# Kernel optimization log

Measured on AMD Instinct MI355X. Metric: run time of the kernel, lower is better.

The kernel has to match this reference:

```python
import jax, jax.numpy as jnp
import numpy as np

B, N_ATOM, N_TOK = 1, 1536, 384
C_ATOM, C_PAIR, C_TOK = 128, 16, 384
C_HID, H, L = 32, 4, 3
HID = 2 * C_ATOM  # n_transition = 2
N_QUERY, N_KEY, INF = 32, 128, 1e9


def _ln(x, gamma=None, beta=None, eps=1e-5):
    mu = jnp.mean(x, axis=-1, keepdims=True)
    var = jnp.mean(jnp.square(x - mu), axis=-1, keepdims=True)
    y = (x - mu) * jax.lax.rsqrt(var + eps)
    if gamma is not None:
        y = y * gamma
    if beta is not None:
        y = y + beta
    return y


def _adaln(a, s, gamma_s, Wg, bg, Ws):
    an = _ln(a)            # LN without affine
    sn = _ln(s, gamma_s)   # scale-only LN
    return jax.nn.sigmoid(sn @ Wg + bg) * an + sn @ Ws


def _block_mask():
    # AtomTransformer.forward: 32-query x 128-key block-local mask
    offset = N_QUERY // 2 - 0.5
    n_center = N_ATOM // N_QUERY + 1
    centers = offset + jnp.arange(n_center, dtype=jnp.float32) * N_QUERY
    idx = jnp.arange(N_ATOM, dtype=jnp.float32)[:, None]
    row = (jnp.abs(idx - centers[None, :]) < N_QUERY / 2).astype(jnp.float32)
    col = (jnp.abs(idx - centers[None, :]) < N_KEY / 2).astype(jnp.float32)
    return (row @ col.T - 1.0) * INF   # [N,N]: 0 in-window, -INF outside


def _forward(ref_pos, ref_mask, ref_element, ref_charge, ref_atom_name_chars,
             ref_space_uid, token_mask, atom_to_token_index,
             W_feats, W_ref_offset, W_inv_sq, W_valid, W_l, W_m,
             W_mlp1, W_mlp2, W_mlp3, W_out_tok,
             attn_ada_gamma_s, attn_ada_Wg, attn_ada_bg, attn_ada_Ws,
             Wq, bq, Wk, Wv, lnz_g, lnz_b, Wb, Wgate, Wo, Wsg, bsg,
             tr_ada_gamma_s, tr_ada_Wg, tr_ada_bg, tr_ada_Ws,
             tr_W1, tr_W2, tr_Wog, tr_bog, tr_Wout):
    # --- RefAtomFeatureEmbedder (AF3 Alg 5 lines 1-6) ---
    feats = jnp.concatenate([
        ref_pos, ref_mask[..., None], ref_element, ref_charge[..., None],
        ref_atom_name_chars.reshape(B, N_ATOM, -1), ref_space_uid[..., None]], axis=-1)
    cl = feats @ W_feats                                     # [B,N,C_ATOM]
    d = ref_pos[:, None, :, :] - ref_pos[:, :, None, :]      # d[l,m] = pos[m]-pos[l]
    v = (ref_space_uid[:, None, :] == ref_space_uid[:, :, None]).astype(jnp.float32)[..., None]
    plm = (d @ W_ref_offset) * v
    inv_sq = 1.0 / (1.0 + jnp.sum(d * d, axis=-1, keepdims=True))
    plm = plm + (inv_sq @ W_inv_sq) * v + (v @ W_valid) * v  # [B,N,N,C_PAIR]
    ql = cl
    # --- single -> pair conditioning + pair MLP ---
    crelu = jax.nn.relu(cl)
    plm = plm + (crelu @ W_l)[:, :, None, :] + (crelu @ W_m)[:, None, :, :]
    h = jax.nn.relu(plm) @ W_mlp1
    h = jax.nn.relu(h) @ W_mlp2
    h = jax.nn.relu(h) @ W_mlp3
    plm = plm + h
    # --- AtomTransformer (Alg 7) -> DiffusionTransformer (Alg 23) ---
    beta = _block_mask()                                     # [N,N]
    atom_mask = jnp.einsum('blt,bt->bl', atom_to_token_index, token_mask)
    mask_bias = (atom_mask - 1.0)[:, None, None, :] * INF    # [B,1,1,N]
    a, s = ql, cl
    inv_sqrt = 1.0 / np.sqrt(C_HID)
    for i in range(L):
        # AttentionPairBias (Alg 24)
        an = _adaln(a, s, attn_ada_gamma_s[i], attn_ada_Wg[i], attn_ada_bg[i], attn_ada_Ws[i])
        q = (an @ Wq[i] + bq[i]).reshape(B, N_ATOM, H, C_HID)
        k = (an @ Wk[i]).reshape(B, N_ATOM, H, C_HID)
        vv = (an @ Wv[i]).reshape(B, N_ATOM, H, C_HID)
        zb = _ln(plm, lnz_g[i], lnz_b[i]) @ Wb[i]            # [B,N,N,H]
        logits = (jnp.einsum('bqhc,bkhc->bhqk', q, k) * inv_sqrt
                  + jnp.moveaxis(zb, -1, 1) + beta[None, None] + mask_bias)
        A = jax.nn.softmax(logits, axis=-1)
        o = jnp.einsum('bhqk,bkhc->bqhc', A, vv)
        g = jax.nn.sigmoid(an @ Wgate[i]).reshape(B, N_ATOM, H, C_HID)
        o = (g * o).reshape(B, N_ATOM, H * C_HID) @ Wo[i]
        attn_out = jax.nn.sigmoid(s @ Wsg[i] + bsg[i]) * o
        # ConditionedTransitionBlock (Alg 25) on pre-attention a (Alg 23)
        tn = _adaln(a, s, tr_ada_gamma_s[i], tr_ada_Wg[i], tr_ada_bg[i], tr_ada_Ws[i])
        hh = jax.nn.silu(tn @ tr_W1[i]) * (tn @ tr_W2[i])
        tr_out = jax.nn.sigmoid(s @ tr_Wog[i] + tr_bog[i]) * (hh @ tr_Wout[i])
        a = attn_out + tr_out
    # --- mean-aggregate atoms -> tokens (Alg 5 line 15) ---
    al = jax.nn.relu(a @ W_out_tok)                          # [B,N,C_TOK]
    counts = jnp.maximum(jnp.sum(atom_to_token_index, axis=1), 1.0)
    a_tok = jnp.einsum('blt,blc->btc', atom_to_token_index, al) / counts[..., None]
    return a_tok


def setup_inputs() -> dict:
    key = jax.random.key(0)
    ks = iter(jax.random.split(key, 80))

    def nrm(shape, scale=0.02):
        return jax.random.normal(next(ks), shape, dtype=jnp.float32) * scale

    inp = {}
    inp['ref_pos'] = jax.random.normal(next(ks), (B, N_ATOM, 3), dtype=jnp.float32) * 3.0
    inp['ref_mask'] = jnp.ones((B, N_ATOM), jnp.float32)
    elem = jax.random.randint(next(ks), (B, N_ATOM), 0, 128)
    inp['ref_element'] = jax.nn.one_hot(elem, 128, dtype=jnp.float32)
    inp['ref_charge'] = jax.random.normal(next(ks), (B, N_ATOM), dtype=jnp.float32)
    chars = jax.random.randint(next(ks), (B, N_ATOM, 4), 0, 64)
    inp['ref_atom_name_chars'] = jax.nn.one_hot(chars, 64, dtype=jnp.float32)
    inp['ref_space_uid'] = jnp.broadcast_to(
        (jnp.arange(N_ATOM) // 8).astype(jnp.float32), (B, N_ATOM))
    inp['token_mask'] = jnp.ones((B, N_TOK), jnp.float32)
    tok = (jnp.arange(N_ATOM) * N_TOK) // N_ATOM  # ~4 atoms per token
    inp['atom_to_token_index'] = jnp.broadcast_to(
        jax.nn.one_hot(tok, N_TOK, dtype=jnp.float32), (B, N_ATOM, N_TOK))
    # embedder params
    inp['W_feats'] = nrm((390, C_ATOM))
    inp['W_ref_offset'] = nrm((3, C_PAIR))
    inp['W_inv_sq'] = nrm((1, C_PAIR))
    inp['W_valid'] = nrm((1, C_PAIR))
    inp['W_l'] = nrm((C_ATOM, C_PAIR))
    inp['W_m'] = nrm((C_ATOM, C_PAIR))
    inp['W_mlp1'] = nrm((C_PAIR, C_PAIR))
    inp['W_mlp2'] = nrm((C_PAIR, C_PAIR))
    inp['W_mlp3'] = nrm((C_PAIR, C_PAIR))
    inp['W_out_tok'] = nrm((C_ATOM, C_TOK))
    # DiffusionTransformer params, stacked over L blocks
    inp['attn_ada_gamma_s'] = jnp.ones((L, C_ATOM), jnp.float32)
    inp['attn_ada_Wg'] = nrm((L, C_ATOM, C_ATOM))
    inp['attn_ada_bg'] = jnp.zeros((L, C_ATOM), jnp.float32)
    inp['attn_ada_Ws'] = nrm((L, C_ATOM, C_ATOM))
    inp['Wq'] = nrm((L, C_ATOM, H * C_HID))
    inp['bq'] = jnp.zeros((L, H * C_HID), jnp.float32)
    inp['Wk'] = nrm((L, C_ATOM, H * C_HID))
    inp['Wv'] = nrm((L, C_ATOM, H * C_HID))
    inp['lnz_g'] = jnp.ones((L, C_PAIR), jnp.float32)
    inp['lnz_b'] = jnp.zeros((L, C_PAIR), jnp.float32)
    inp['Wb'] = nrm((L, C_PAIR, H))
    inp['Wgate'] = nrm((L, C_ATOM, H * C_HID))
    inp['Wo'] = nrm((L, H * C_HID, C_ATOM))
    inp['Wsg'] = nrm((L, C_ATOM, C_ATOM))
    inp['bsg'] = jnp.full((L, C_ATOM), -2.0, jnp.float32)
    inp['tr_ada_gamma_s'] = jnp.ones((L, C_ATOM), jnp.float32)
    inp['tr_ada_Wg'] = nrm((L, C_ATOM, C_ATOM))
    inp['tr_ada_bg'] = jnp.zeros((L, C_ATOM), jnp.float32)
    inp['tr_ada_Ws'] = nrm((L, C_ATOM, C_ATOM))
    inp['tr_W1'] = nrm((L, C_ATOM, HID))
    inp['tr_W2'] = nrm((L, C_ATOM, HID))
    inp['tr_Wog'] = nrm((L, C_ATOM, C_ATOM))
    inp['tr_bog'] = jnp.full((L, C_ATOM), -2.0, jnp.float32)
    inp['tr_Wout'] = nrm((L, HID, C_ATOM))
    return inp


def reference(ref_pos, ref_mask, ref_element, ref_charge, ref_atom_name_chars,
              ref_space_uid, token_mask, atom_to_token_index,
              W_feats, W_ref_offset, W_inv_sq, W_valid, W_l, W_m,
              W_mlp1, W_mlp2, W_mlp3, W_out_tok,
              attn_ada_gamma_s, attn_ada_Wg, attn_ada_bg, attn_ada_Ws,
              Wq, bq, Wk, Wv, lnz_g, lnz_b, Wb, Wgate, Wo, Wsg, bsg,
              tr_ada_gamma_s, tr_ada_Wg, tr_ada_bg, tr_ada_Ws,
              tr_W1, tr_W2, tr_Wog, tr_bog, tr_Wout):
    return _forward(ref_pos, ref_mask, ref_element, ref_charge, ref_atom_name_chars,
                    ref_space_uid, token_mask, atom_to_token_index,
                    W_feats, W_ref_offset, W_inv_sq, W_valid, W_l, W_m,
                    W_mlp1, W_mlp2, W_mlp3, W_out_tok,
                    attn_ada_gamma_s, attn_ada_Wg, attn_ada_bg, attn_ada_Ws,
                    Wq, bq, Wk, Wv, lnz_g, lnz_b, Wb, Wgate, Wo, Wsg, bsg,
                    tr_ada_gamma_s, tr_ada_Wg, tr_ada_bg, tr_ada_Ws,
                    tr_W1, tr_W2, tr_Wog, tr_bog, tr_Wout)
```

## Files before the change

kernel.cpp:

```cpp
#include <hip/hip_runtime.h>
#include <math.h>

#define N_ATOM 1536
#define NLAYER 3
#define NC     196608L
#define ZSTRIDE 786432L

struct GD { const float* A; const float* B; float* C; const float* ks; const float* bias;
            const float* sg; const float* ad; int act; int ldb; int ldc; int mode; };
struct GB { GD g[18]; };

__global__ __launch_bounds__(128) void embed_tok_kernel(
    const float* __restrict__ pos, const float* __restrict__ rmask,
    const float* __restrict__ elem, const float* __restrict__ charge,
    const float* __restrict__ chars, const float* __restrict__ uid,
    const float* __restrict__ Wf, const float* __restrict__ W_l, const float* __restrict__ W_m,
    const float* __restrict__ a2t, const float* __restrict__ tmask,
    float* __restrict__ cl, float* __restrict__ aa,
    float* __restrict__ pl, float* __restrict__ pm,
    int* __restrict__ tok, float* __restrict__ amask)
{
  int l = blockIdx.x, c = threadIdx.x;
  __shared__ int sidx[6];
  __shared__ float crow[128];
  if (elem[(long)l * 128 + c] > 0.5f) sidx[0] = c;
  float v0 = chars[(long)l * 256 + c];
  if (v0 > 0.5f) sidx[1 + (c >> 6)] = c & 63;
  float v1 = chars[(long)l * 256 + 128 + c];
  if (v1 > 0.5f) sidx[3 + (c >> 6)] = c & 63;
  for (int j = c; j < 384; j += 128)
    if (a2t[(long)l * 384 + j] > 0.5f) sidx[5] = j;
  __syncthreads();
  float acc = pos[l * 3 + 0] * Wf[c]
            + pos[l * 3 + 1] * Wf[128 + c]
            + pos[l * 3 + 2] * Wf[256 + c]
            + rmask[l] * Wf[384 + c]
            + Wf[(4 + sidx[0]) * 128 + c]
            + charge[l] * Wf[132 * 128 + c]
            + Wf[(133 + sidx[1]) * 128 + c]
            + Wf[(197 + sidx[2]) * 128 + c]
            + Wf[(261 + sidx[3]) * 128 + c]
            + Wf[(325 + sidx[4]) * 128 + c]
            + uid[l] * Wf[389 * 128 + c];
  long gi = (long)l * 128 + c;
  cl[gi] = acc; aa[gi] = acc; crow[c] = fmaxf(acc, 0.f);
  __syncthreads();
  if (c < 32) {
    const float* W = (c < 16) ? W_l : W_m;
    int o = c & 15;
    float s = 0.f;
    for (int cc = 0; cc < 128; cc++) s = fmaf(crow[cc], W[cc * 16 + o], s);
    if (c < 16) pl[l * 16 + o] = s; else pm[l * 16 + o] = s;
  }
  if (c == 127) {
    int j = sidx[5];
    tok[l] = j; amask[l] = tmask[j];
  }
}

__device__ __forceinline__ void gemm64_body(float* sm, const GD d, int row0, int col0) {
  float* As = sm; float* Bs = sm + 2176;
  float* rmu = sm + 4352;
  float* rsd = sm + 4416;
  int tid = threadIdx.x;
  if (d.mode >= 1) {
    int r = tid >> 2, sgi = tid & 3;
    const float* Ar = d.A + (long)(row0 + r) * 128 + sgi * 32;
    float4 vv[8];
    float s1 = 0.f;
#pragma unroll
    for (int c4 = 0; c4 < 8; c4++) {
      vv[c4] = *(const float4*)(Ar + c4 * 4);
      s1 += vv[c4].x + vv[c4].y + vv[c4].z + vv[c4].w;
    }
    s1 += __shfl_xor(s1, 1); s1 += __shfl_xor(s1, 2);
    float mu = s1 * (1.f / 128.f);
    float s2 = 0.f;
#pragma unroll
    for (int c4 = 0; c4 < 8; c4++) {
      float dx = vv[c4].x - mu, dy = vv[c4].y - mu, dz = vv[c4].z - mu, dw = vv[c4].w - mu;
      s2 += dx * dx + dy * dy + dz * dz + dw * dw;
    }
    s2 += __shfl_xor(s2, 1); s2 += __shfl_xor(s2, 2);
    if (sgi == 0) {
      rmu[r] = mu;
      rsd[r] = rsqrtf(s2 * (1.f / 128.f) + 1e-5f);
    }
  }
  int tx = tid & 15, ty = tid >> 4;
  float acc[4][4] = {};
  for (int k0 = 0; k0 < 128; k0 += 32) {
    __syncthreads();
    { int r = tid >> 3, k4 = tid & 7;
#pragma unroll
      for (int half = 0; half < 2; half++) {
        int row = r + half * 32;
        long gro = (long)(row0 + row) * 128 + k0 + k4 * 4;
        float4 v = *(const float4*)(d.A + gro);
        float vals[4] = {v.x, v.y, v.z, v.w};
        if (d.mode >= 1) {
          float mu = rmu[row], sd = rsd[row];
          if (d.mode == 2) {
            float4 sg4 = *(const float4*)(d.sg + gro);
            float4 ad4 = *(const float4*)(d.ad + gro);
            vals[0] = fmaf(sg4.x, (vals[0] - mu) * sd, ad4.x);
            vals[1] = fmaf(sg4.y, (vals[1] - mu) * sd, ad4.y);
            vals[2] = fmaf(sg4.z, (vals[2] - mu) * sd, ad4.z);
            vals[3] = fmaf(sg4.w, (vals[3] - mu) * sd, ad4.w);
          } else {
#pragma unroll
            for (int cc = 0; cc < 4; cc++) vals[cc] = (vals[cc] - mu) * sd;
          }
        }
        if (d.ks) {
          const float* kp = d.ks + k0 + k4 * 4;
#pragma unroll
          for (int cc = 0; cc < 4; cc++) vals[cc] *= kp[cc];
        }
        As[(k4 * 4 + 0) * 68 + row] = vals[0]; As[(k4 * 4 + 1) * 68 + row] = vals[1];
        As[(k4 * 4 + 2) * 68 + row] = vals[2]; As[(k4 * 4 + 3) * 68 + row] = vals[3];
      } }
    { int kk = tid >> 4, n4 = tid & 15;
#pragma unroll
      for (int half = 0; half < 2; half++) {
        int k = kk + half * 16;
        *(float4*)&Bs[k * 68 + n4 * 4] = *(const float4*)(d.B + (long)(k0 + k) * d.ldb + col0 + n4 * 4);
      } }
    __syncthreads();
#pragma unroll
    for (int kk = 0; kk < 32; kk++) {
      float4 a = *(const float4*)&As[kk * 68 + ty * 4];
      float4 b = *(const float4*)&Bs[kk * 68 + tx * 4];
      float av[4] = {a.x, a.y, a.z, a.w}, bv[4] = {b.x, b.y, b.z, b.w};
#pragma unroll
      for (int i = 0; i < 4; i++)
#pragma unroll
        for (int j = 0; j < 4; j++) acc[i][j] = fmaf(av[i], bv[j], acc[i][j]);
    }
  }
  __syncthreads();
#pragma unroll
  for (int i = 0; i < 4; i++) {
    int row = row0 + ty * 4 + i;
#pragma unroll
    for (int j = 0; j < 4; j++) {
      int col = col0 + tx * 4 + j;
      float x = acc[i][j];
      if (d.bias) x += d.bias[col];
      if (d.act == 1) x = 1.f / (1.f + expf(-x));
      else if (d.act == 2) x = fmaxf(x, 0.f);
      d.C[(long)row * d.ldc + col] = x;
    }
  }
}

__global__ __launch_bounds__(256) void gemm64(GB args)
{
  __shared__ __align__(16) float sm[4480];
  gemm64_body(sm, args.g[blockIdx.z], blockIdx.y * 64, blockIdx.x * 64);
}

__global__ __launch_bounds__(256) void zpre_kernel(
    const float* __restrict__ pos, const float* __restrict__ uid,
    const float* __restrict__ Wro, const float* __restrict__ Winv, const float* __restrict__ Wval,
    const float* __restrict__ M1, const float* __restrict__ M2, const float* __restrict__ M3,
    const float* __restrict__ Lg, const float* __restrict__ Lb, const float* __restrict__ Wb,
    const float* __restrict__ pl, const float* __restrict__ pm, float* __restrict__ zb,
    GB ba)
{
  __shared__ __align__(16) float sm[4480];
  int bid = blockIdx.x, tid = threadIdx.x;
  if (bid >= 768) {
    int u = bid - 768;
    GD d = ba.g[u / 48];
    int tt = u % 48;
    gemm64_body(sm, d, (tt >> 1) * 64, (tt & 1) * 64);
    return;
  }
  if (tid < 48)  sm[tid] = Wro[tid];
  if (tid < 16)  { sm[48 + tid] = Winv[tid]; sm[64 + tid] = Wval[tid]; }
  sm[80 + tid] = M1[tid]; sm[336 + tid] = M2[tid]; sm[592 + tid] = M3[tid];
  if (tid < 48)  { sm[848 + tid] = Lg[tid]; sm[896 + tid] = Lb[tid]; }
  if (tid < 192) sm[944 + tid] = Wb[tid];
  __syncthreads();
  const float* sWro = sm;      const float* sWinv = sm + 48;  const float* sWval = sm + 64;
  const float* sM1 = sm + 80;  const float* sM2 = sm + 336;   const float* sM3 = sm + 592;
  const float* sLg = sm + 848; const float* sLb = sm + 896;   const float* sWb = sm + 944;
  int b = bid >> 4;
  int pc = (bid & 15) * 256 + tid;
  int qi = pc >> 7, kj = pc & 127;
  int l = b * 32 + qi, m = b * 32 - 48 + kj;
  long base = (long)(b * 32 + qi) * 128 + kj;
  if (m < 0 || m >= N_ATOM) {
    for (int i = 0; i < NLAYER; i++)
      for (int h = 0; h < 4; h++) zb[i * ZSTRIDE + h * NC + base] = 0.f;
    return;
  }
  float dx = pos[m * 3 + 0] - pos[l * 3 + 0];
  float dy = pos[m * 3 + 1] - pos[l * 3 + 1];
  float dz = pos[m * 3 + 2] - pos[l * 3 + 2];
  float v = (uid[m] == uid[l]) ? 1.f : 0.f;
  float inv = 1.f / (1.f + dx * dx + dy * dy + dz * dz);
  float pv[16], ha[16], hb[16];
#pragma unroll
  for (int j = 0; j < 16; j++)
    pv[j] = v * (dx * sWro[j] + dy * sWro[16 + j] + dz * sWro[32 + j] + inv * sWinv[j] + sWval[j])
            + pl[l * 16 + j] + pm[m * 16 + j];
#pragma unroll
  for (int jo = 0; jo < 16; jo++) { float s = 0.f; for (int ji = 0; ji < 16; ji++) s = fmaf(fmaxf(pv[ji], 0.f), sM1[ji * 16 + jo], s); ha[jo] = s; }
#pragma unroll
  for (int jo = 0; jo < 16; jo++) { float s = 0.f; for (int ji = 0; ji < 16; ji++) s = fmaf(fmaxf(ha[ji], 0.f), sM2[ji * 16 + jo], s); hb[jo] = s; }
#pragma unroll
  for (int jo = 0; jo < 16; jo++) { float s = 0.f; for (int ji = 0; ji < 16; ji++) s = fmaf(fmaxf(hb[ji], 0.f), sM3[ji * 16 + jo], s); ha[jo] = s; }
#pragma unroll
  for (int j = 0; j < 16; j++) pv[j] += ha[j];
  for (int i = 0; i < NLAYER; i++) {
    float mu = 0.f;
#pragma unroll
    for (int j = 0; j < 16; j++) mu += pv[j];
    mu *= (1.f / 16.f);
    float var = 0.f;
#pragma unroll
    for (int j = 0; j < 16; j++) { float dd = pv[j] - mu; var += dd * dd; }
    var *= (1.f / 16.f);
    float rs = rsqrtf(var + 1e-5f);
    float zn[16];
#pragma unroll
    for (int j = 0; j < 16; j++) zn[j] = (pv[j] - mu) * rs * sLg[i * 16 + j] + sLb[i * 16 + j];
    for (int h = 0; h < 4; h++) {
      float s = 0.f;
#pragma unroll
      for (int j = 0; j < 16; j++) s = fmaf(zn[j], sWb[i * 64 + j * 4 + h], s);
      zb[i * ZSTRIDE + h * NC + base] = s;
    }
  }
}

__global__ __launch_bounds__(256) void attn_tr_kernel(
    const float* __restrict__ qb, const float* __restrict__ kb, const float* __restrict__ vb,
    const float* __restrict__ gb, const float* __restrict__ zb, const float* __restrict__ amask,
    float* __restrict__ go,
    const float* __restrict__ h1, const float* __restrict__ h2, const float* __restrict__ B2,
    const float* __restrict__ g2, float* __restrict__ trbuf)
{
  __shared__ __align__(16) float sm[11904];
  int bid = blockIdx.x, t = threadIdx.x;
  if (bid >= 384) {
    int u = bid - 384;
    int row0 = (u >> 1) * 32, col0 = (u & 1) * 64;
    float* As = sm; float* Bs = sm + 1152;
    int tx = t & 15, ty = t >> 4;
    float acc2[2][4] = {};
    for (int k0 = 0; k0 < 256; k0 += 32) {
      __syncthreads();
      { int r = t >> 3, k4 = t & 7;
        long o = (long)(row0 + r) * 256 + k0 + k4 * 4;
        float4 x = *(const float4*)(h1 + o);
        float4 y = *(const float4*)(h2 + o);
        As[(k4 * 4 + 0) * 36 + r] = (x.x / (1.f + expf(-x.x))) * y.x;
        As[(k4 * 4 + 1) * 36 + r] = (x.y / (1.f + expf(-x.y))) * y.y;
        As[(k4 * 4 + 2) * 36 + r] = (x.z / (1.f + expf(-x.z))) * y.z;
        As[(k4 * 4 + 3) * 36 + r] = (x.w / (1.f + expf(-x.w))) * y.w;
      }
      for (int e = t; e < 512; e += 256) {
        int k = e >> 4, n4 = e & 15;
        *(float4*)&Bs[k * 68 + n4 * 4] = *(const float4*)(B2 + (long)(k0 + k) * 128 + col0 + n4 * 4);
      }
      __syncthreads();
#pragma unroll
      for (int kk = 0; kk < 32; kk++) {
        float a0 = As[kk * 36 + ty * 2], a1 = As[kk * 36 + ty * 2 + 1];
        float4 b = *(const float4*)&Bs[kk * 68 + tx * 4];
        float bv[4] = {b.x, b.y, b.z, b.w};
#pragma unroll
        for (int j = 0; j < 4; j++) {
          acc2[0][j] = fmaf(a0, bv[j], acc2[0][j]);
          acc2[1][j] = fmaf(a1, bv[j], acc2[1][j]);
        }
      }
    }
#pragma unroll
    for (int i = 0; i < 2; i++) {
      long o = (long)(row0 + ty * 2 + i) * 128 + col0 + tx * 4;
      float4 g4 = *(const float4*)(g2 + o);
      float4 r;
      r.x = g4.x * acc2[i][0]; r.y = g4.y * acc2[i][1];
      r.z = g4.z * acc2[i][2]; r.w = g4.w * acc2[i][3];
      *(float4*)(trbuf + o) = r;
    }
    return;
  }
  float* qs = sm;
  float* ks = sm + 576;
  float* vs = sm + 5184;
  float* ps = sm + 9792;
  int h = bid / 96, bx = bid - h * 96;
  int b = bx >> 1, half = bx & 1;
  int q0 = b * 32 + half * 16;
  int kbase = b * 32 - 48;
  const float* zbh = zb + (long)h * NC;
  if (t < 128) {
    int qi = t >> 3, c4 = t & 7;
    *(float4*)&qs[qi * 36 + c4 * 4] = *(const float4*)(qb + (long)(q0 + qi) * 128 + h * 32 + c4 * 4);
  }
  for (int idx = t; idx < 128 * 8; idx += 256) {
    int kj = idx >> 3, c4 = idx & 7;
    int m = kbase + kj;
    float4 kv = make_float4(0.f, 0.f, 0.f, 0.f), vv = make_float4(0.f, 0.f, 0.f, 0.f);
    if (m >= 0 && m < N_ATOM) {
      kv = *(const float4*)(kb + (long)m * 128 + h * 32 + c4 * 4);
      vv = *(const float4*)(vb + (long)m * 128 + h * 32 + c4 * 4);
    }
    *(float4*)&ks[kj * 36 + c4 * 4] = kv;
    *(float4*)&vs[kj * 36 + c4 * 4] = vv;
  }
  __syncthreads();
  const float isq = 0.17677669529663687f;
  for (int p = t; p < 2048; p += 256) {
    int qi = p >> 7, kj = p & 127;
    int m = kbase + kj;
    float s = 0.f;
#pragma unroll
    for (int c4 = 0; c4 < 8; c4++) {
      float4 a = *(const float4*)&qs[qi * 36 + c4 * 4];
      float4 k4 = *(const float4*)&ks[kj * 36 + c4 * 4];
      s = fmaf(a.x, k4.x, s); s = fmaf(a.y, k4.y, s);
      s = fmaf(a.z, k4.z, s); s = fmaf(a.w, k4.w, s);
    }
    float logit;
    if (m >= 0 && m < N_ATOM) {
      logit = s * isq + zbh[(long)(q0 + qi) * 128 + kj] + (amask[m] - 1.f) * 1e9f;
    } else {
      logit = -1e9f;
    }
    ps[qi * 132 + kj] = logit;
  }
  __syncthreads();
  {
    int row = t >> 4, ln = t & 15;
    float mx = -1e30f;
    for (int kj = ln; kj < 128; kj += 16) mx = fmaxf(mx, ps[row * 132 + kj]);
#pragma unroll
    for (int o = 8; o > 0; o >>= 1) mx = fmaxf(mx, __shfl_xor(mx, o));
    float smv = 0.f;
    for (int kj = ln; kj < 128; kj += 16) { float e = expf(ps[row * 132 + kj] - mx); ps[row * 132 + kj] = e; smv += e; }
#pragma unroll
    for (int o = 8; o > 0; o >>= 1) smv += __shfl_xor(smv, o);
    float r = 1.f / smv;
    for (int kj = ln; kj < 128; kj += 16) ps[row * 132 + kj] *= r;
  }
  __syncthreads();
  {
    int qi = t >> 4, seg = (t >> 3) & 1, c4 = t & 7;
    float4 acc = make_float4(0.f, 0.f, 0.f, 0.f);
    int kj0 = seg * 64;
#pragma unroll 4
    for (int kj = kj0; kj < kj0 + 64; kj++) {
      float p = ps[qi * 132 + kj];
      float4 v = *(const float4*)&vs[kj * 36 + c4 * 4];
      acc.x = fmaf(p, v.x, acc.x); acc.y = fmaf(p, v.y, acc.y);
      acc.z = fmaf(p, v.z, acc.z); acc.w = fmaf(p, v.w, acc.w);
    }
    acc.x += __shfl_xor(acc.x, 8);
    acc.y += __shfl_xor(acc.y, 8);
    acc.z += __shfl_xor(acc.z, 8);
    acc.w += __shfl_xor(acc.w, 8);
    if (seg == 0) {
      long gi = (long)(q0 + qi) * 128 + h * 32 + c4 * 4;
      float4 g = *(const float4*)(gb + gi);
      acc.x *= g.x; acc.y *= g.y; acc.z *= g.z; acc.w *= g.w;
      *(float4*)(go + gi) = acc;
    }
  }
}

__global__ __launch_bounds__(256) void wo_kernel(
    const float* __restrict__ A1, const float* __restrict__ B1,
    const float* __restrict__ g1, const float* __restrict__ tr,
    float* __restrict__ C)
{
  __shared__ __align__(16) float As[32 * 36];
  __shared__ __align__(16) float Bs[32 * 68];
  const int N = 128;
  int t = threadIdx.x;
  int row0 = blockIdx.y * 32, col0 = blockIdx.x * 64;
  int tx = t & 15, ty = t >> 4;
  float acc1[2][4] = {};
  for (int k0 = 0; k0 < 128; k0 += 32) {
    __syncthreads();
    { int r = t >> 3, k4 = t & 7;
      float4 v = *(const float4*)(A1 + (long)(row0 + r) * 128 + k0 + k4 * 4);
      As[(k4 * 4 + 0) * 36 + r] = v.x; As[(k4 * 4 + 1) * 36 + r] = v.y;
      As[(k4 * 4 + 2) * 36 + r] = v.z; As[(k4 * 4 + 3) * 36 + r] = v.w;
    }
    for (int e = t; e < 512; e += 256) {
      int k = e >> 4, n4 = e & 15;
      *(float4*)&Bs[k * 68 + n4 * 4] = *(const float4*)(B1 + (long)(k0 + k) * N + col0 + n4 * 4);
    }
    __syncthreads();
#pragma unroll
    for (int kk = 0; kk < 32; kk++) {
      float a0 = As[kk * 36 + ty * 2], a1 = As[kk * 36 + ty * 2 + 1];
      float4 b = *(const float4*)&Bs[kk * 68 + tx * 4];
      float bv[4] = {b.x, b.y, b.z, b.w};
#pragma unroll
      for (int j = 0; j < 4; j++) {
        acc1[0][j] = fmaf(a0, bv[j], acc1[0][j]);
        acc1[1][j] = fmaf(a1, bv[j], acc1[1][j]);
      }
    }
  }
#pragma unroll
  for (int i = 0; i < 2; i++) {
    long o = (long)(row0 + ty * 2 + i) * N + col0 + tx * 4;
    float4 ga = *(const float4*)(g1 + o);
    float4 tv = *(const float4*)(tr + o);
    float4 r;
    r.x = ga.x * acc1[i][0] + tv.x;
    r.y = ga.y * acc1[i][1] + tv.y;
    r.z = ga.z * acc1[i][2] + tv.z;
    r.w = ga.w * acc1[i][3] + tv.w;
    *(float4*)(C + o) = r;
  }
}

__global__ __launch_bounds__(256) void gemm_scatter(
    const float* __restrict__ A, const float* __restrict__ B,
    const int* __restrict__ tok,
    float* __restrict__ out, int K)
{
  __shared__ __align__(16) float As[32][68];
  __shared__ __align__(16) float Bs[32][68];
  int tid = threadIdx.x;
  int row0 = blockIdx.y * 64, col0 = blockIdx.x * 64;
  int tx = tid & 15, ty = tid >> 4;
  float acc[4][4] = {};
  for (int k0 = 0; k0 < K; k0 += 32) {
    __syncthreads();
    { int r = tid >> 3, k4 = tid & 7;
#pragma unroll
      for (int half = 0; half < 2; half++) {
        int row = r + half * 32;
        float4 v = *(const float4*)(A + (long)(row0 + row) * K + k0 + k4 * 4);
        As[k4 * 4 + 0][row] = v.x; As[k4 * 4 + 1][row] = v.y;
        As[k4 * 4 + 2][row] = v.z; As[k4 * 4 + 3][row] = v.w;
      } }
    { int kk = tid >> 4, n4 = tid & 15;
#pragma unroll
      for (int half = 0; half < 2; half++) {
        int k = kk + half * 16;
        float4 v = *(const float4*)(B + (long)(k0 + k) * 384 + col0 + n4 * 4);
        *(float4*)&Bs[k][n4 * 4] = v;
      } }
    __syncthreads();
#pragma unroll
    for (int kk = 0; kk < 32; kk++) {
      float4 a = *(const float4*)&As[kk][ty * 4];
      float4 b = *(const float4*)&Bs[kk][tx * 4];
      float av[4] = {a.x, a.y, a.z, a.w}, bv[4] = {b.x, b.y, b.z, b.w};
#pragma unroll
      for (int i = 0; i < 4; i++)
#pragma unroll
        for (int j = 0; j < 4; j++) acc[i][j] = fmaf(av[i], bv[j], acc[i][j]);
    }
  }
  __syncthreads();
  int r0 = row0 + ty * 4;
  int t0 = tok[r0];
  int cnt = 0;
#pragma unroll
  for (int i = 0; i < 4; i++) cnt += (tok[r0 + i] == t0) ? 1 : 0;
  float inv = 1.f / fmaxf((float)cnt, 1.f);
#pragma unroll
  for (int j = 0; j < 4; j++) {
    int col = col0 + tx * 4 + j;
    float s = 0.f;
#pragma unroll
    for (int i = 0; i < 4; i++)
      if (tok[r0 + i] == t0) s += fmaxf(acc[i][j], 0.f);
    out[(long)t0 * 384 + col] = s * inv;
  }
}

extern "C" void kernel_launch(void* const* d_in, const int* in_sizes, int n_in,
                              void* d_out, int out_size, void* d_ws, size_t ws_size,
                              hipStream_t stream)
{
  const float* pos    = (const float*)d_in[0];
  const float* rmask  = (const float*)d_in[1];
  const float* elem   = (const float*)d_in[2];
  const float* charge = (const float*)d_in[3];
  const float* chars  = (const float*)d_in[4];
  const float* uid    = (const float*)d_in[5];
  const float* tmask  = (const float*)d_in[6];
  const float* a2t    = (const float*)d_in[7];
  const float* Wf     = (const float*)d_in[8];
  const float* Wro    = (const float*)d_in[9];
  const float* Winv   = (const float*)d_in[10];
  const float* Wval   = (const float*)d_in[11];
  const float* W_l    = (const float*)d_in[12];
  const float* W_m    = (const float*)d_in[13];
  const float* M1     = (const float*)d_in[14];
  const float* M2     = (const float*)d_in[15];
  const float* M3     = (const float*)d_in[16];
  const float* Wtok   = (const float*)d_in[17];
  const float* gA     = (const float*)d_in[18];
  const float* WgA    = (const float*)d_in[19];
  const float* bgA    = (const float*)d_in[20];
  const float* WsA    = (const float*)d_in[21];
  const float* Wq     = (const float*)d_in[22];
  const float* bq     = (const float*)d_in[23];
  const float* Wk     = (const float*)d_in[24];
  const float* Wv     = (const float*)d_in[25];
  const float* Lg     = (const float*)d_in[26];
  const float* Lb     = (const float*)d_in[27];
  const float* Wb     = (const float*)d_in[28];
  const float* Wgate  = (const float*)d_in[29];
  const float* Wo     = (const float*)d_in[30];
  const float* Wsg    = (const float*)d_in[31];
  const float* bsg    = (const float*)d_in[32];
  const float* gT     = (const float*)d_in[33];
  const float* WgT    = (const float*)d_in[34];
  const float* bgT    = (const float*)d_in[35];
  const float* WsT    = (const float*)d_in[36];
  const float* trW1   = (const float*)d_in[37];
  const float* trW2   = (const float*)d_in[38];
  const float* Wog    = (const float*)d_in[39];
  const float* bog    = (const float*)d_in[40];
  const float* Wout   = (const float*)d_in[41];
  float* out = (float*)d_out;

  float* ws = (float*)d_ws;
  size_t off = 0;
  auto alloc = [&](size_t n) { float* p = ws + off; off += n; return p; };
  float* cl     = alloc(NC);
  float* aa     = alloc(NC);
  float* qbuf   = alloc(NC);
  float* kbuf   = alloc(NC);
  float* vbuf   = alloc(NC);
  float* gbuf   = alloc(NC);
  float* gobuf  = alloc(NC);
  float* trbuf  = alloc(NC);
  float* h1     = alloc((size_t)N_ATOM * 256);
  float* h2     = alloc((size_t)N_ATOM * 256);
  float* pl     = alloc((size_t)N_ATOM * 16);
  float* pm     = alloc((size_t)N_ATOM * 16);
  float* zbias  = alloc((size_t)NLAYER * ZSTRIDE);
  float* sgA    = alloc(NC * NLAYER);
  float* adA    = alloc(NC * NLAYER);
  float* sgT    = alloc(NC * NLAYER);
  float* adT    = alloc(NC * NLAYER);
  float* gsg    = alloc(NC * NLAYER);
  float* gog    = alloc(NC * NLAYER);
  float* amask  = alloc(N_ATOM);
  int*   tok    = (int*)alloc(N_ATOM);
  (void)ws_size; (void)in_sizes; (void)n_in; (void)out_size;

  embed_tok_kernel<<<N_ATOM, 128, 0, stream>>>(pos, rmask, elem, charge, chars, uid, Wf,
                                               W_l, W_m, a2t, tmask,
                                               cl, aa, pl, pm, tok, amask);

  {
    GB ba = {};
    for (int i = 0; i < NLAYER; i++) {
      size_t o = (size_t)i * NC;
      ba.g[i * 6 + 0] = { cl, WgA + i * 16384, sgA + o, gA + i * 128, bgA + i * 128, nullptr, nullptr, 1, 128, 128, 1 };
      ba.g[i * 6 + 1] = { cl, WsA + i * 16384, adA + o, gA + i * 128, nullptr,       nullptr, nullptr, 0, 128, 128, 1 };
      ba.g[i * 6 + 2] = { cl, WgT + i * 16384, sgT + o, gT + i * 128, bgT + i * 128, nullptr, nullptr, 1, 128, 128, 1 };
      ba.g[i * 6 + 3] = { cl, WsT + i * 16384, adT + o, gT + i * 128, nullptr,       nullptr, nullptr, 0, 128, 128, 1 };
      ba.g[i * 6 + 4] = { cl, Wsg + i * 16384, gsg + o, nullptr,      bsg + i * 128, nullptr, nullptr, 1, 128, 128, 0 };
      ba.g[i * 6 + 5] = { cl, Wog + i * 16384, gog + o, nullptr,      bog + i * 128, nullptr, nullptr, 1, 128, 128, 0 };
    }
    zpre_kernel<<<768 + 864, 256, 0, stream>>>(pos, uid, Wro, Winv, Wval, M1, M2, M3,
                                               Lg, Lb, Wb, pl, pm, zbias, ba);
  }

  for (int i = 0; i < NLAYER; i++) {
    size_t o = (size_t)i * NC;
    {
      GB ba = {};
      ba.g[0] = { aa, Wq + i * 16384,        qbuf,     nullptr, bq + i * 128, sgA + o, adA + o, 0, 128, 128, 2 };
      ba.g[1] = { aa, Wk + i * 16384,        kbuf,     nullptr, nullptr,      sgA + o, adA + o, 0, 128, 128, 2 };
      ba.g[2] = { aa, Wv + i * 16384,        vbuf,     nullptr, nullptr,      sgA + o, adA + o, 0, 128, 128, 2 };
      ba.g[3] = { aa, Wgate + i * 16384,     gbuf,     nullptr, nullptr,      sgA + o, adA + o, 1, 128, 128, 2 };
      ba.g[4] = { aa, trW1 + i * 32768,       h1,      nullptr, nullptr,      sgT + o, adT + o, 0, 256, 256, 2 };
      ba.g[5] = { aa, trW1 + i * 32768 + 128, h1 + 128, nullptr, nullptr,     sgT + o, adT + o, 0, 256, 256, 2 };
      ba.g[6] = { aa, trW2 + i * 32768,       h2,      nullptr, nullptr,      sgT + o, adT + o, 0, 256, 256, 2 };
      ba.g[7] = { aa, trW2 + i * 32768 + 128, h2 + 128, nullptr, nullptr,     sgT + o, adT + o, 0, 256, 256, 2 };
      gemm64<<<dim3(2, 24, 8), 256, 0, stream>>>(ba);
    }
    attn_tr_kernel<<<480, 256, 0, stream>>>(qbuf, kbuf, vbuf, gbuf,
                                            zbias + (size_t)i * ZSTRIDE, amask, gobuf,
                                            h1, h2, Wout + i * 32768, gog + o, trbuf);
    wo_kernel<<<dim3(2, 48), 256, 0, stream>>>(gobuf, Wo + i * 16384, gsg + o, trbuf, aa);
  }

  gemm_scatter<<<dim3(6, 24), 256, 0, stream>>>(aa, Wtok, tok, out, 128);
}
```

Before: 326.3 us.

## Fuse Wo projection into attention kernel via atomics and defer residual combine

```diff
diff --git a/kernel.cpp b/kernel.cpp
--- a/kernel.cpp
+++ b/kernel.cpp
@@ -7,7 +7,8 @@
 #define ZSTRIDE 786432L
 
 struct GD { const float* A; const float* B; float* C; const float* ks; const float* bias;
-            const float* sg; const float* ad; int act; int ldb; int ldc; int mode; };
+            const float* sg; const float* ad; const float* g1; const float* t2;
+            int act; int ldb; int ldc; int mode; };
 struct GB { GD g[18]; };
 
 __global__ __launch_bounds__(128) void embed_tok_kernel(
@@ -58,6 +59,17 @@
   }
 }
 
+__device__ __forceinline__ float4 ldA(const GD& d, long gro) {
+  float4 v = *(const float4*)(d.A + gro);
+  if (d.mode == 3) {
+    float4 g = *(const float4*)(d.g1 + gro);
+    float4 t = *(const float4*)(d.t2 + gro);
+    v.x = fmaf(g.x, v.x, t.x); v.y = fmaf(g.y, v.y, t.y);
+    v.z = fmaf(g.z, v.z, t.z); v.w = fmaf(g.w, v.w, t.w);
+  }
+  return v;
+}
+
 __device__ __forceinline__ void gemm64_body(float* sm, const GD d, int row0, int col0) {
   float* As = sm; float* Bs = sm + 2176;
   float* rmu = sm + 4352;
@@ -65,12 +77,12 @@
   int tid = threadIdx.x;
   if (d.mode >= 1) {
     int r = tid >> 2, sgi = tid & 3;
-    const float* Ar = d.A + (long)(row0 + r) * 128 + sgi * 32;
+    long rowbase = (long)(row0 + r) * 128 + sgi * 32;
     float4 vv[8];
     float s1 = 0.f;
 #pragma unroll
     for (int c4 = 0; c4 < 8; c4++) {
-      vv[c4] = *(const float4*)(Ar + c4 * 4);
+      vv[c4] = ldA(d, rowbase + c4 * 4);
       s1 += vv[c4].x + vv[c4].y + vv[c4].z + vv[c4].w;
     }
     s1 += __shfl_xor(s1, 1); s1 += __shfl_xor(s1, 2);
@@ -96,11 +108,11 @@
       for (int half = 0; half < 2; half++) {
         int row = r + half * 32;
         long gro = (long)(row0 + row) * 128 + k0 + k4 * 4;
-        float4 v = *(const float4*)(d.A + gro);
+        float4 v = ldA(d, gro);
         float vals[4] = {v.x, v.y, v.z, v.w};
         if (d.mode >= 1) {
           float mu = rmu[row], sd = rsd[row];
-          if (d.mode == 2) {
+          if (d.mode >= 2) {
             float4 sg4 = *(const float4*)(d.sg + gro);
             float4 ad4 = *(const float4*)(d.ad + gro);
             vals[0] = fmaf(sg4.x, (vals[0] - mu) * sd, ad4.x);
@@ -239,7 +251,7 @@
 __global__ __launch_bounds__(256) void attn_tr_kernel(
     const float* __restrict__ qb, const float* __restrict__ kb, const float* __restrict__ vb,
     const float* __restrict__ gb, const float* __restrict__ zb, const float* __restrict__ amask,
-    float* __restrict__ go,
+    const float* __restrict__ Wo, float* __restrict__ Sacc,
     const float* __restrict__ h1, const float* __restrict__ h2, const float* __restrict__ B2,
     const float* __restrict__ g2, float* __restrict__ trbuf)
 {
@@ -369,65 +381,41 @@
       long gi = (long)(q0 + qi) * 128 + h * 32 + c4 * 4;
       float4 g = *(const float4*)(gb + gi);
       acc.x *= g.x; acc.y *= g.y; acc.z *= g.z; acc.w *= g.w;
-      *(float4*)(go + gi) = acc;
-    }
-  }
-}
-
-__global__ __launch_bounds__(256) void wo_kernel(
-    const float* __restrict__ A1, const float* __restrict__ B1,
-    const float* __restrict__ g1, const float* __restrict__ tr,
-    float* __restrict__ C)
-{
-  __shared__ __align__(16) float As[32 * 36];
-  __shared__ __align__(16) float Bs[32 * 68];
-  const int N = 128;
-  int t = threadIdx.x;
-  int row0 = blockIdx.y * 32, col0 = blockIdx.x * 64;
-  int tx = t & 15, ty = t >> 4;
-  float acc1[2][4] = {};
-  for (int k0 = 0; k0 < 128; k0 += 32) {
-    __syncthreads();
-    { int r = t >> 3, k4 = t & 7;
-      float4 v = *(const float4*)(A1 + (long)(row0 + r) * 128 + k0 + k4 * 4);
-      As[(k4 * 4 + 0) * 36 + r] = v.x; As[(k4 * 4 + 1) * 36 + r] = v.y;
-      As[(k4 * 4 + 2) * 36 + r] = v.z; As[(k4 * 4 + 3) * 36 + r] = v.w;
-    }
-    for (int e = t; e < 512; e += 256) {
-      int k = e >> 4, n4 = e & 15;
-      *(float4*)&Bs[k * 68 + n4 * 4] = *(const float4*)(B1 + (long)(k0 + k) * N + col0 + n4 * 4);
-    }
-    __syncthreads();
-#pragma unroll
-    for (int kk = 0; kk < 32; kk++) {
-      float a0 = As[kk * 36 + ty * 2], a1 = As[kk * 36 + ty * 2 + 1];
-      float4 b = *(const float4*)&Bs[kk * 68 + tx * 4];
-      float bv[4] = {b.x, b.y, b.z, b.w};
-#pragma unroll
-      for (int j = 0; j < 4; j++) {
-        acc1[0][j] = fmaf(a0, bv[j], acc1[0][j]);
-        acc1[1][j] = fmaf(a1, bv[j], acc1[1][j]);
-      }
-    }
-  }
-#pragma unroll
-  for (int i = 0; i < 2; i++) {
-    long o = (long)(row0 + ty * 2 + i) * N + col0 + tx * 4;
-    float4 ga = *(const float4*)(g1 + o);
-    float4 tv = *(const float4*)(tr + o);
-    float4 r;
-    r.x = ga.x * acc1[i][0] + tv.x;
-    r.y = ga.y * acc1[i][1] + tv.y;
-    r.z = ga.z * acc1[i][2] + tv.z;
-    r.w = ga.w * acc1[i][3] + tv.w;
-    *(float4*)(C + o) = r;
+      *(float4*)&qs[qi * 36 + c4 * 4] = acc;
+    }
+  }
+  {
+    const float* WoH = Wo + (long)h * 32 * 128;
+    for (int e = t; e < 1024; e += 256)
+      *(float4*)&ks[e * 4] = *(const float4*)(WoH + e * 4);
+  }
+  __syncthreads();
+  {
+    int qi = t >> 4, n0 = (t & 15) * 8;
+    float p0[8] = {};
+    const float* w_s = ks;
+#pragma unroll 4
+    for (int c = 0; c < 32; c++) {
+      float ov = qs[qi * 36 + c];
+      const float* wr = w_s + c * 128 + n0;
+      float4 w0 = *(const float4*)wr;
+      float4 w1 = *(const float4*)(wr + 4);
+      p0[0] = fmaf(ov, w0.x, p0[0]); p0[1] = fmaf(ov, w0.y, p0[1]);
+      p0[2] = fmaf(ov, w0.z, p0[2]); p0[3] = fmaf(ov, w0.w, p0[3]);
+      p0[4] = fmaf(ov, w1.x, p0[4]); p0[5] = fmaf(ov, w1.y, p0[5]);
+      p0[6] = fmaf(ov, w1.z, p0[6]); p0[7] = fmaf(ov, w1.w, p0[7]);
+    }
+    float* dst = Sacc + (long)(q0 + qi) * 128 + n0;
+#pragma unroll
+    for (int j = 0; j < 8; j++) atomicAdd(dst + j, p0[j]);
   }
 }
 
 __global__ __launch_bounds__(256) void gemm_scatter(
-    const float* __restrict__ A, const float* __restrict__ B,
+    const float* __restrict__ S2, const float* __restrict__ T2, const float* __restrict__ G2,
+    const float* __restrict__ B,
     const int* __restrict__ tok,
-    float* __restrict__ out, int K)
+    float* __restrict__ out)
 {
   __shared__ __align__(16) float As[32][68];
   __shared__ __align__(16) float Bs[32][68];
@@ -435,13 +423,18 @@
   int row0 = blockIdx.y * 64, col0 = blockIdx.x * 64;
   int tx = tid & 15, ty = tid >> 4;
   float acc[4][4] = {};
-  for (int k0 = 0; k0 < K; k0 += 32) {
+  for (int k0 = 0; k0 < 128; k0 += 32) {
     __syncthreads();
     { int r = tid >> 3, k4 = tid & 7;
 #pragma unroll
       for (int half = 0; half < 2; half++) {
         int row = r + half * 32;
-        float4 v = *(const float4*)(A + (long)(row0 + row) * K + k0 + k4 * 4);
+        long o = (long)(row0 + row) * 128 + k0 + k4 * 4;
+        float4 v = *(const float4*)(S2 + o);
+        float4 g = *(const float4*)(G2 + o);
+        float4 tv = *(const float4*)(T2 + o);
+        v.x = fmaf(g.x, v.x, tv.x); v.y = fmaf(g.y, v.y, tv.y);
+        v.z = fmaf(g.z, v.z, tv.z); v.w = fmaf(g.w, v.w, tv.w);
         As[k4 * 4 + 0][row] = v.x; As[k4 * 4 + 1][row] = v.y;
         As[k4 * 4 + 2][row] = v.z; As[k4 * 4 + 3][row] = v.w;
       } }
@@ -449,8 +442,7 @@
 #pragma unroll
       for (int half = 0; half < 2; half++) {
         int k = kk + half * 16;
-        float4 v = *(const float4*)(B + (long)(k0 + k) * 384 + col0 + n4 * 4);
-        *(float4*)&Bs[k][n4 * 4] = v;
+        *(float4*)&Bs[k][n4 * 4] = *(const float4*)(B + (long)(k0 + k) * 384 + col0 + n4 * 4);
       } }
     __syncthreads();
 #pragma unroll
@@ -539,7 +531,7 @@
   float* kbuf   = alloc(NC);
   float* vbuf   = alloc(NC);
   float* gbuf   = alloc(NC);
-  float* gobuf  = alloc(NC);
+  float* Sbuf   = alloc(NC * NLAYER);
   float* trbuf  = alloc(NC);
   float* h1     = alloc((size_t)N_ATOM * 256);
   float* h2     = alloc((size_t)N_ATOM * 256);
@@ -556,6 +548,8 @@
   int*   tok    = (int*)alloc(N_ATOM);
   (void)ws_size; (void)in_sizes; (void)n_in; (void)out_size;
 
+  hipMemsetAsync(Sbuf, 0, sizeof(float) * NC * NLAYER, stream);
+
   embed_tok_kernel<<<N_ATOM, 128, 0, stream>>>(pos, rmask, elem, charge, chars, uid, Wf,
                                                W_l, W_m, a2t, tmask,
                                                cl, aa, pl, pm, tok, amask);
@@ -564,13 +558,14 @@
     GB ba = {};
     for (int i = 0; i < NLAYER; i++) {
       size_t o = (size_t)i * NC;
-      ba.g[i * 6 + 0] = { cl, WgA + i * 16384, sgA + o, gA + i * 128, bgA + i * 128, nullptr, nullptr, 1, 128, 128, 1 };
-      ba.g[i * 6 + 1] = { cl, WsA + i * 16384, adA + o, gA + i * 128, nullptr,       nullptr, nullptr, 0, 128, 128, 1 };
-      ba.g[i * 6 + 2] = { cl, WgT + i * 16384, sgT + o, gT + i * 128, bgT + i * 128, nullptr, nullptr, 1, 128, 128, 1 };
-      ba.g[i * 6 + 3] = { cl, WsT + i * 16384, adT + o, gT + i * 128, nullptr,       nullptr, nullptr, 0, 128, 128, 1 };
-      ba.g[i * 6 + 4] = { cl, Wsg + i * 16384, gsg + o, nullptr,      bsg + i * 128, nullptr, nullptr, 1, 128, 128, 0 };
-      ba.g[i * 6 + 5] = { cl, Wog + i * 16384, gog + o, nullptr,      bog + i * 128, nullptr, nullptr, 1, 128, 128, 0 };
-    }
+      ba.g[i * 6 + 0] = { cl, WgA + i * 16384, sgA + o, gA + i * 128, bgA + i * 128, nullptr, nullptr, nullptr, nullptr, 1, 128, 128, 1 };
+      ba.g[i * 6 + 1] = { cl, WsA + i * 16384, adA + o, gA + i * 128, nullptr,       nullptr, nullptr, nullptr, nullptr, 0, 128, 128, 1 };
+      ba.g[i * 6 + 2] = { cl, WgT + i * 16384, sgT + o, gT + i * 128, bgT + i * 128, nullptr, nullptr, nullptr, nullptr, 1, 128, 128, 1 };
+      ba.g[i * 6 + 3] = { cl, WsT + i * 16384, adT + o, gT + i * 128, nullptr,       nullptr, nullptr, nullptr, nullptr, 0, 128, 128, 1 };
+      ba.g[i * 6 + 4] = { cl, Wsg + i * 16384, gsg + o, nullptr,      bsg + i * 128, nullptr, nullptr, nullptr, nullptr, 1, 128, 128, 1 | 0 };
+      ba.g[i * 6 + 5] = { cl, Wog + i * 16384, gog + o, nullptr,      bog + i * 128, nullptr, nullptr, nullptr, nullptr, 1, 128, 128, 0 };
+    }
+    for (int i = 0; i < NLAYER; i++) ba.g[i * 6 + 4].mode = 0;
     zpre_kernel<<<768 + 864, 256, 0, stream>>>(pos, uid, Wro, Winv, Wval, M1, M2, M3,
                                                Lg, Lb, Wb, pl, pm, zbias, ba);
   }
@@ -579,21 +574,37 @@
     size_t o = (size_t)i * NC;
     {
       GB ba = {};
-      ba.g[0] = { aa, Wq + i * 16384,        qbuf,     nullptr, bq + i * 128, sgA + o, adA + o, 0, 128, 128, 2 };
-      ba.g[1] = { aa, Wk + i * 16384,        kbuf,     nullptr, nullptr,      sgA + o, adA + o, 0, 128, 128, 2 };
-      ba.g[2] = { aa, Wv + i * 16384,        vbuf,     nullptr, nullptr,      sgA + o, adA + o, 0, 128, 128, 2 };
-      ba.g[3] = { aa, Wgate + i * 16384,     gbuf,     nullptr, nullptr,      sgA + o, adA + o, 1, 128, 128, 2 };
-      ba.g[4] = { aa, trW1 + i * 32768,       h1,      nullptr, nullptr,      sgT + o, adT + o, 0, 256, 256, 2 };
-      ba.g[5] = { aa, trW1 + i * 32768 + 128, h1 + 128, nullptr, nullptr,     sgT + o, adT + o, 0, 256, 256, 2 };
-      ba.g[6] = { aa, trW2 + i * 32768,       h2,      nullptr, nullptr,      sgT + o, adT + o, 0, 256, 256, 2 };
-      ba.g[7] = { aa, trW2 + i * 32768 + 128, h2 + 128, nullptr, nullptr,     sgT + o, adT + o, 0, 256, 256, 2 };
+      for (int s = 0; s < 8; s++) {
+        GD& d = ba.g[s];
+        if (i == 0) { d.A = aa; d.g1 = nullptr; d.t2 = nullptr; d.mode = 2; }
+        else {
+          d.A = Sbuf + (size_t)(i - 1) * NC;
+          d.g1 = gsg + (size_t)(i - 1) * NC;
+          d.t2 = trbuf;
+          d.mode = 3;
+        }
+        d.ks = nullptr; d.bias = nullptr; d.act = 0;
+        if (s < 4) { d.sg = sgA + o; d.ad = adA + o; d.ldb = 128; d.ldc = 128; }
+        else       { d.sg = sgT + o; d.ad = adT + o; d.ldb = 256; d.ldc = 256; }
+        switch (s) {
+          case 0: d.B = Wq + i * 16384;          d.C = qbuf;     d.bias = bq + i * 128; break;
+          case 1: d.B = Wk + i * 16384;          d.C = kbuf;     break;
+          case 2: d.B = Wv + i * 16384;          d.C = vbuf;     break;
+          case 3: d.B = Wgate + i * 16384;       d.C = gbuf;     d.act = 1; break;
+          case 4: d.B = trW1 + i * 32768;        d.C = h1;       break;
+          case 5: d.B = trW1 + i * 32768 + 128;  d.C = h1 + 128; break;
+          case 6: d.B = trW2 + i * 32768;        d.C = h2;       break;
+          default:d.B = trW2 + i * 32768 + 128;  d.C = h2 + 128; break;
+        }
+      }
       gemm64<<<dim3(2, 24, 8), 256, 0, stream>>>(ba);
     }
     attn_tr_kernel<<<480, 256, 0, stream>>>(qbuf, kbuf, vbuf, gbuf,
-                                            zbias + (size_t)i * ZSTRIDE, amask, gobuf,
+                                            zbias + (size_t)i * ZSTRIDE, amask,
+                                            Wo + i * 16384, Sbuf + o,
                                             h1, h2, Wout + i * 32768, gog + o, trbuf);
-    wo_kernel<<<dim3(2, 48), 256, 0, stream>>>(gobuf, Wo + i * 16384, gsg + o, trbuf, aa);
-  }
-
-  gemm_scatter<<<dim3(6, 24), 256, 0, stream>>>(aa, Wtok, tok, out, 128);
-}
+  }
+
+  gemm_scatter<<<dim3(6, 24), 256, 0, stream>>>(Sbuf + (size_t)2 * NC, trbuf, gsg + (size_t)2 * NC,
+                                                Wtok, tok, out);
+}
```

New measurement: 358.8 us. 1.1x slower.
